# Optimization experiments

Hardware: AMD Instinct MI355X
Metric: run time of the kernel (lower is better)

## Reference

```python
import jax, jax.numpy as jnp
import numpy as np

T, B, IN, OUT = 32, 16, 64, 64
L, W, S = 4096, 64, 3          # mem_length, mem_width, shifting_size
READ_SIZE = W + 3 + S           # k, beta, g, gamma, s
WRITE_SIZE = W + 3 + S + 2 * W  # addressing params + erase + add


def setup_inputs() -> dict:
    key = jax.random.key(0)
    k1, k2 = jax.random.split(key)
    inputs = jax.random.normal(k1, (T, B, IN), dtype=jnp.float32)
    Wc = jax.random.normal(k2, (IN + OUT + W, OUT + READ_SIZE + WRITE_SIZE), dtype=jnp.float32) * 0.05
    bc = jnp.zeros((OUT + READ_SIZE + WRITE_SIZE,), dtype=jnp.float32)
    return {"inputs": inputs, "Wc": Wc, "bc": bc}


def _get_w(params, w_prev, memory):
    # params: [B, W+3+S]; w_prev: [B, L]; memory: [B, L, W]
    k = params[:, :W]
    beta = jax.nn.softplus(params[:, W])[:, None]
    g = jax.nn.sigmoid(params[:, W + 1])[:, None]
    gamma = jax.nn.softplus(params[:, W + 2])[:, None] + 1.0
    s = jax.nn.softmax(params[:, -S:], axis=-1)
    eps = 1e-14
    norm_k = jnp.sqrt(jnp.sum(k * k, axis=-1, keepdims=True) + eps)    # [B,1]
    norm_mem = jnp.sqrt(jnp.sum(memory * memory, axis=-1) + eps)       # [B,L]
    K = jnp.einsum('blw,bw->bl', memory, k) / (norm_mem * norm_k)      # cosine sim
    w_c = jax.nn.softmax(K * beta, axis=-1)
    w_g = w_c * g + (1.0 - g) * w_prev
    # circular shift: w_tilde[i] = sum_j s[j] * w_g[(i + j - left) mod L]
    left = S // 2
    shifted = jnp.stack([jnp.roll(w_g, left - j, axis=1) for j in range(S)], axis=-1)  # [B,L,S]
    w_tilde = jnp.einsum('bls,bs->bl', shifted, s)
    w = jnp.power(w_tilde, gamma)   # sharpen, gamma >= 1
    return w / jnp.sum(w, axis=1, keepdims=True)


def reference(inputs, Wc, bc):
    Bsz = inputs.shape[1]
    r0 = jnp.zeros((Bsz, W), jnp.float32)
    o0 = jnp.zeros((Bsz, OUT), jnp.float32)
    w0 = jnp.zeros((Bsz, L), jnp.float32).at[:, 0].set(1.0)  # one-hot init weights
    m0 = jnp.zeros((Bsz, L, W), jnp.float32)

    def step(carry, x_t):
        r, out, rw, ww, mem = carry
        co = jnp.concatenate([x_t, out, r], axis=1) @ Wc + bc  # linear controller
        out = co[:, :OUT]
        rp = co[:, OUT:OUT + READ_SIZE]
        wp = co[:, -WRITE_SIZE:]
        # read head (uses pre-write memory)
        rw = _get_w(rp, rw, mem)
        r = jnp.einsum('blw,bl->bw', mem, rw)
        # write head: address with same memory, then erase/add
        ww = _get_w(wp[:, :-2 * W], ww, mem)
        e = jax.nn.sigmoid(wp[:, -2 * W:-W])
        a = wp[:, -W:]
        mem = mem * (1.0 - ww[:, :, None] * e[:, None, :]) + ww[:, :, None] * a[:, None, :]
        return (r, out, rw, ww, mem), out

    _, outs = jax.lax.scan(step, (r0, o0, w0, w0, m0), inputs)
    return outs  # [T, B, OUT]
```

## Files before the change

### kernel.cpp

```cpp
#include <hip/hip_runtime.h>

#define T_STEPS 32
#define BATCH   16
#define NBPB    8
#define NBLK    (BATCH * NBPB)
#define NTHR    1024
#define LSL     512
#define MSTR    65
#define NIN     192
#define CO      332

#define OFF_CTR   0
#define OFF_SSUM  512
#define OFF_RSUM  (OFF_SSUM + BATCH * T_STEPS * 4)
#define OFF_HE    (OFF_RSUM + BATCH * T_STEPS * 64)
#define OFF_HP    (OFF_HE + BATCH * T_STEPS * NBPB * 4)
#define COMM_FLOATS (OFF_HP + BATCH * (T_STEPS + 1) * NBPB * 4)

__device__ __forceinline__ float waveSum(float v) {
#pragma unroll
  for (int off = 32; off > 0; off >>= 1) v += __shfl_xor(v, off, 64);
  return v;
}
__device__ __forceinline__ float sigmoidf(float x) { return 1.f / (1.f + __expf(-x)); }
__device__ __forceinline__ float softplusf(float x) { return x > 15.f ? x : log1pf(__expf(x)); }
__device__ __forceinline__ float aload(const float* p) {
  return __hip_atomic_load(p, __ATOMIC_RELAXED, __HIP_MEMORY_SCOPE_AGENT);
}
__device__ __forceinline__ void astore(float* p, float v) {
  __hip_atomic_store(p, v, __ATOMIC_RELAXED, __HIP_MEMORY_SCOPE_AGENT);
}

__device__ __forceinline__ void gbar(unsigned* c, unsigned expected) {
  __syncthreads();
  if (threadIdx.x == 0) {
    atomicAdd(c, 1u);
    while (__hip_atomic_load(c, __ATOMIC_RELAXED, __HIP_MEMORY_SCOPE_AGENT) < expected)
      __builtin_amdgcn_s_sleep(2);
  }
  __syncthreads();
}

__global__ void __launch_bounds__(NTHR, 1) ntm_kernel(
    const float* __restrict__ inp, const float* __restrict__ Wc,
    const float* __restrict__ bcv, float* __restrict__ dout,
    float* __restrict__ comm)
{
  const int b   = blockIdx.x >> 3;
  const int g   = blockIdx.x & 7;
  const int tid = threadIdx.x;
  const int wv  = tid >> 6;
  const int lane = tid & 63;

  __shared__ float mem[LSL * MSTR];
  __shared__ float wpR[LSL], wpW[LSL];
  __shared__ float wbR[LSL], wbW[LSL];
  __shared__ float erR[LSL], erW[LSL];
  __shared__ float xin[NIN], kr[64], kw[64], psc[12], elds[64], alds[64];
  __shared__ float outb[2][64], scrA[8], scrB[8], red[8], rpart[64], edge[8];

  unsigned* ctr = (unsigned*)comm + b * 32;

  for (int i = tid; i < LSL * MSTR; i += NTHR) mem[i] = 0.f;
  if (tid < LSL) { wpR[tid] = 0.f; wpW[tid] = 0.f; }
  if (g == 0 && tid == 0) { wpR[0] = 1.f; wpW[0] = 1.f; }
  if (tid < 64) { outb[0][tid] = 0.f; outb[1][tid] = 0.f; }
  {
    float* hp0 = comm + OFF_HP + ((size_t)(b * (T_STEPS + 1) + 0) * NBPB + g) * 4;
    if (tid == 0)       { float v = (g == 0) ? 1.f : 0.f; astore(hp0 + 0, v); astore(hp0 + 2, v); }
    if (tid == LSL - 1) { astore(hp0 + 1, 0.f); astore(hp0 + 3, 0.f); }
  }
  unsigned expct = NBPB;
  gbar(ctr, expct);

  for (int t = 0; t < T_STEPS; ++t) {
    float* sS  = comm + OFF_SSUM + (size_t)(b * T_STEPS + t) * 4;
    float* rS  = comm + OFF_RSUM + (size_t)(b * T_STEPS + t) * 64;
    float* hE  = comm + OFF_HE + ((size_t)(b * T_STEPS + t) * NBPB + g) * 4;
    float* hPn = comm + OFF_HP + ((size_t)(b * (T_STEPS + 1) + t + 1) * NBPB + g) * 4;

    if (tid < 64)       xin[tid] = inp[((size_t)t * BATCH + b) * 64 + tid];
    else if (tid < 128) xin[tid] = outb[(t + 1) & 1][tid - 64];
    else if (tid < 192) xin[tid] = (t == 0) ? 0.f
                        : aload(comm + OFF_RSUM + (size_t)(b * T_STEPS + t - 1) * 64 + (tid - 128));
    __syncthreads();

    if (tid < 2 * CO) {
      const int col = tid >> 1, h = tid & 1;
      float acc = h ? 0.f : bcv[col];
      const float* wcp = Wc + col + (size_t)(96 * h) * CO;
#pragma unroll 8
      for (int i = 0; i < 96; ++i) acc = fmaf(xin[96 * h + i], wcp[(size_t)i * CO], acc);
      acc += __shfl_xor(acc, 1, 64);
      if (h == 0) {
        if (col < 64) {
          outb[t & 1][col] = acc;
          if (g == 0) dout[((size_t)t * BATCH + b) * 64 + col] = acc;
        }
        else if (col < 128) kr[col - 64] = acc;
        else if (col < 134) psc[col - 128] = acc;
        else if (col < 198) kw[col - 134] = acc;
        else if (col < 204) psc[6 + (col - 198)] = acc;
        else if (col < 268) elds[col - 204] = sigmoidf(acc);
        else                alds[col - 268] = acc;
      }
    }
    __syncthreads();
    if (wv == 0)      { float v = kr[lane]; float s = waveSum(v * v); if (!lane) red[4] = 1.f / sqrtf(s + 1e-14f); }
    else if (wv == 1) { float v = kw[lane]; float s = waveSum(v * v); if (!lane) red[5] = 1.f / sqrtf(s + 1e-14f); }
    __syncthreads();

    {
      float sRl = 0.f, sWl = 0.f;
      if (tid < LSL) {
        const float invnkR = red[4], betaR = softplusf(psc[0]);
        const float invnkW = red[5], betaW = softplusf(psc[6]);
        float ss = 0.f, dr = 0.f, dw = 0.f;
        const int base = tid * MSTR;
#pragma unroll 8
        for (int w = 0; w < 64; ++w) {
          float v = mem[base + w];
          ss = fmaf(v, v, ss); dr = fmaf(v, kr[w], dr); dw = fmaf(v, kw[w], dw);
        }
        float rinv = rsqrtf(ss + 1e-14f);
        float eRv = __expf(betaR * (dr * rinv * invnkR - 1.f));
        float eWv = __expf(betaW * (dw * rinv * invnkW - 1.f));
        erR[tid] = eRv; erW[tid] = eWv;
        if (tid == 0)       { astore(hE + 0, eRv); astore(hE + 2, eWv); }
        if (tid == LSL - 1) { astore(hE + 1, eRv); astore(hE + 3, eWv); }
        sRl = eRv; sWl = eWv;
      }
      sRl = waveSum(sRl); sWl = waveSum(sWl);
      if (!lane && wv < 8) { scrA[wv] = sRl; scrB[wv] = sWl; }
      __syncthreads();
      if (tid == 0) {
        float a = 0.f, bb = 0.f;
        for (int j = 0; j < 8; ++j) { a += scrA[j]; bb += scrB[j]; }
        atomicAdd(sS + 0, a); atomicAdd(sS + 1, bb);
      }
    }
    expct += NBPB; gbar(ctr, expct);

    {
      const int gm = (g + NBPB - 1) & 7, gp = (g + 1) & 7;
      const float* hEm = comm + OFF_HE + ((size_t)(b * T_STEPS + t) * NBPB + gm) * 4;
      const float* hEp = comm + OFF_HE + ((size_t)(b * T_STEPS + t) * NBPB + gp) * 4;
      const float* hPm = comm + OFF_HP + ((size_t)(b * (T_STEPS + 1) + t) * NBPB + gm) * 4;
      const float* hPp = comm + OFF_HP + ((size_t)(b * (T_STEPS + 1) + t) * NBPB + gp) * 4;
      if (tid == 0) { red[0] = 1.f / aload(sS + 0); red[1] = 1.f / aload(sS + 1); }
      if (tid == 1) { edge[0] = aload(hEm + 1); edge[1] = aload(hEm + 3);
                      edge[2] = aload(hPm + 1); edge[3] = aload(hPm + 3); }
      if (tid == 2) { edge[4] = aload(hEp + 0); edge[5] = aload(hEp + 2);
                      edge[6] = aload(hPp + 0); edge[7] = aload(hPp + 2); }
      __syncthreads();

      float pRl = 0.f, pWl = 0.f;
      if (tid < LSL) {
        const float invSR = red[0], invSW = red[1];
        float gR = sigmoidf(psc[1]), gaR = softplusf(psc[2]) + 1.f;
        float x0 = psc[3], x1 = psc[4], x2 = psc[5];
        float mx = fmaxf(x0, fmaxf(x1, x2));
        float e0 = __expf(x0 - mx), e1 = __expf(x1 - mx), e2 = __expf(x2 - mx);
        float es = 1.f / (e0 + e1 + e2);
        float sr0 = e0 * es, sr1 = e1 * es, sr2 = e2 * es;
        float gW = sigmoidf(psc[7]), gaW = softplusf(psc[8]) + 1.f;
        float y0 = psc[9], y1 = psc[10], y2 = psc[11];
        float my = fmaxf(y0, fmaxf(y1, y2));
        float f0 = __expf(y0 - my), f1 = __expf(y1 - my), f2 = __expf(y2 - my);
        float fs = 1.f / (f0 + f1 + f2);
        float sw0 = f0 * fs, sw1 = f1 * fs, sw2 = f2 * fs;
        const float aR = gR * invSR, bR = 1.f - gR;
        const float aW = gW * invSW, bW = 1.f - gW;

        float erm = tid ? erR[tid - 1] : edge[0];
        float ewm = tid ? erW[tid - 1] : edge[1];
        float prm = tid ? wpR[tid - 1] : edge[2];
        float pwm = tid ? wpW[tid - 1] : edge[3];
        float erp = (tid < LSL - 1) ? erR[tid + 1] : edge[4];
        float ewp = (tid < LSL - 1) ? erW[tid + 1] : edge[5];
        float prp = (tid < LSL - 1) ? wpR[tid + 1] : edge[6];
        float pwp = (tid < LSL - 1) ? wpW[tid + 1] : edge[7];

        float wgm = aR * erm + bR * prm;
        float wg0 = aR * erR[tid] + bR * wpR[tid];
        float wgp = aR * erp + bR * prp;
        float wR = __powf(sr0 * wgm + sr1 * wg0 + sr2 * wgp, gaR);
        float vgm = aW * ewm + bW * pwm;
        float vg0 = aW * erW[tid] + bW * wpW[tid];
        float vgp = aW * ewp + bW * pwp;
        float wW = __powf(sw0 * vgm + sw1 * vg0 + sw2 * vgp, gaW);
        wbR[tid] = wR; wbW[tid] = wW;
        pRl = wR; pWl = wW;
      }
      pRl = waveSum(pRl); pWl = waveSum(pWl);
      if (!lane && wv < 8) { scrA[wv] = pRl; scrB[wv] = pWl; }
      __syncthreads();
      if (tid == 0) {
        float a = 0.f, bb = 0.f;
        for (int j = 0; j < 8; ++j) { a += scrA[j]; bb += scrB[j]; }
        atomicAdd(sS + 2, a); atomicAdd(sS + 3, bb);
      }
    }
    expct += NBPB; gbar(ctr, expct);

    {
      if (tid == 0) { red[2] = 1.f / aload(sS + 2); red[3] = 1.f / aload(sS + 3); }
      __syncthreads();
      if (tid < LSL) {
        float nR = wbR[tid] * red[2];
        float nW = wbW[tid] * red[3];
        wpR[tid] = nR; wpW[tid] = nW;
        if (tid == 0)       { astore(hPn + 0, nR); astore(hPn + 2, nW); }
        if (tid == LSL - 1) { astore(hPn + 1, nR); astore(hPn + 3, nW); }
      }
      __syncthreads();

      float rwv[8], wwv[8];
#pragma unroll
      for (int k = 0; k < 8; ++k) { rwv[k] = wpR[lane + 64 * k]; wwv[k] = wpW[lane + 64 * k]; }
#pragma unroll
      for (int r2 = 0; r2 < 4; ++r2) {
        const int w = wv * 4 + r2;
        const float e_w = elds[w], a_w = alds[w];
        float racc = 0.f;
#pragma unroll
        for (int k = 0; k < 8; ++k) {
          const int idx = (lane + 64 * k) * MSTR + w;
          float v = mem[idx];
          racc = fmaf(v, rwv[k], racc);
          float nv = fmaf(v, -(wwv[k] * e_w), v);
          mem[idx] = fmaf(wwv[k], a_w, nv);
        }
        racc = waveSum(racc);
        if (!lane) rpart[w] = racc;
      }
      __syncthreads();
      if (tid < 64) atomicAdd(rS + tid, rpart[tid]);
    }
    expct += NBPB; gbar(ctr, expct);
  }
}

extern "C" void kernel_launch(void* const* d_in, const int* in_sizes, int n_in,
                              void* d_out, int out_size, void* d_ws, size_t ws_size,
                              hipStream_t stream) {
  const float* inp = (const float*)d_in[0];
  const float* Wc  = (const float*)d_in[1];
  const float* bcv = (const float*)d_in[2];
  float* dout = (float*)d_out;
  float* comm = (float*)d_ws;

  hipMemsetAsync(comm, 0, (size_t)COMM_FLOATS * sizeof(float), stream);

  void* args[] = { (void*)&inp, (void*)&Wc, (void*)&bcv, (void*)&dout, (void*)&comm };
  hipLaunchCooperativeKernel((void*)ntm_kernel, dim3(NBLK), dim3(NTHR),
                             args, 0, stream);
}
```

Measured before the change: 753.8 us.

## Move read-vector reduction before normalization to drop one grid barrier per step

The read vector is now computed from the unnormalized sharpened weights during the second phase and divided by the global sum in the next step's controller input, which removes the third grid barrier per timestep. The similarity pass splits each row across two threads so all 1024 threads participate, and the scalar gate/shift coefficients are computed once by a single thread and broadcast through shared memory. The block-to-(batch, slice) mapping is transposed and the barrier spin sleep is shortened. The memory update now runs without a barrier after it, relying on the next step's barriers for ordering, which is a subtle correctness risk.

```diff
diff --git a/kernel.cpp b/kernel.cpp
--- a/kernel.cpp
+++ b/kernel.cpp
@@ -36,7 +36,7 @@
   if (threadIdx.x == 0) {
     atomicAdd(c, 1u);
     while (__hip_atomic_load(c, __ATOMIC_RELAXED, __HIP_MEMORY_SCOPE_AGENT) < expected)
-      __builtin_amdgcn_s_sleep(2);
+      __builtin_amdgcn_s_sleep(1);
   }
   __syncthreads();
 }
@@ -46,8 +46,8 @@
     const float* __restrict__ bcv, float* __restrict__ dout,
     float* __restrict__ comm)
 {
-  const int b   = blockIdx.x >> 3;
-  const int g   = blockIdx.x & 7;
+  const int b   = blockIdx.x & 15;
+  const int g   = blockIdx.x >> 4;
   const int tid = threadIdx.x;
   const int wv  = tid >> 6;
   const int lane = tid & 63;
@@ -57,7 +57,8 @@
   __shared__ float wbR[LSL], wbW[LSL];
   __shared__ float erR[LSL], erW[LSL];
   __shared__ float xin[NIN], kr[64], kw[64], psc[12], elds[64], alds[64];
-  __shared__ float outb[2][64], scrA[8], scrB[8], red[8], rpart[64], edge[8];
+  __shared__ float outb[2][64], scrA[16], scrB[16], red[8], rpart[64];
+  __shared__ float edge[8], coef[12];
 
   unsigned* ctr = (unsigned*)comm + b * 32;
 
@@ -81,8 +82,14 @@
 
     if (tid < 64)       xin[tid] = inp[((size_t)t * BATCH + b) * 64 + tid];
     else if (tid < 128) xin[tid] = outb[(t + 1) & 1][tid - 64];
-    else if (tid < 192) xin[tid] = (t == 0) ? 0.f
-                        : aload(comm + OFF_RSUM + (size_t)(b * T_STEPS + t - 1) * 64 + (tid - 128));
+    else if (tid < 192) {
+      if (t == 0) xin[tid] = 0.f;
+      else {
+        const float* sP = comm + OFF_SSUM + (size_t)(b * T_STEPS + t - 1) * 4;
+        const float* rP = comm + OFF_RSUM + (size_t)(b * T_STEPS + t - 1) * 64;
+        xin[tid] = aload(rP + (tid - 128)) / aload(sP + 2);
+      }
+    }
     __syncthreads();
 
     if (tid < 2 * CO) {
@@ -108,34 +115,40 @@
     __syncthreads();
     if (wv == 0)      { float v = kr[lane]; float s = waveSum(v * v); if (!lane) red[4] = 1.f / sqrtf(s + 1e-14f); }
     else if (wv == 1) { float v = kw[lane]; float s = waveSum(v * v); if (!lane) red[5] = 1.f / sqrtf(s + 1e-14f); }
+    else if (wv == 2 && !lane) { red[6] = softplusf(psc[0]); red[7] = softplusf(psc[6]); }
     __syncthreads();
 
     {
-      float sRl = 0.f, sWl = 0.f;
-      if (tid < LSL) {
-        const float invnkR = red[4], betaR = softplusf(psc[0]);
-        const float invnkW = red[5], betaW = softplusf(psc[6]);
-        float ss = 0.f, dr = 0.f, dw = 0.f;
-        const int base = tid * MSTR;
+      const float invnkR = red[4], invnkW = red[5];
+      const float betaR = red[6], betaW = red[7];
+      const int l = tid >> 1, h = tid & 1;
+      const int base = l * MSTR + 32 * h;
+      const float* krh = kr + 32 * h;
+      const float* kwh = kw + 32 * h;
+      float ss = 0.f, dr = 0.f, dw = 0.f;
 #pragma unroll 8
-        for (int w = 0; w < 64; ++w) {
-          float v = mem[base + w];
-          ss = fmaf(v, v, ss); dr = fmaf(v, kr[w], dr); dw = fmaf(v, kw[w], dw);
-        }
-        float rinv = rsqrtf(ss + 1e-14f);
-        float eRv = __expf(betaR * (dr * rinv * invnkR - 1.f));
-        float eWv = __expf(betaW * (dw * rinv * invnkW - 1.f));
-        erR[tid] = eRv; erW[tid] = eWv;
-        if (tid == 0)       { astore(hE + 0, eRv); astore(hE + 2, eWv); }
-        if (tid == LSL - 1) { astore(hE + 1, eRv); astore(hE + 3, eWv); }
-        sRl = eRv; sWl = eWv;
-      }
+      for (int i = 0; i < 32; ++i) {
+        float v = mem[base + i];
+        ss = fmaf(v, v, ss); dr = fmaf(v, krh[i], dr); dw = fmaf(v, kwh[i], dw);
+      }
+      ss += __shfl_xor(ss, 1, 64);
+      dr += __shfl_xor(dr, 1, 64);
+      dw += __shfl_xor(dw, 1, 64);
+      float rinv = rsqrtf(ss + 1e-14f);
+      float eRv = __expf(betaR * (dr * rinv * invnkR - 1.f));
+      float eWv = __expf(betaW * (dw * rinv * invnkW - 1.f));
+      if (h == 0) {
+        erR[l] = eRv; erW[l] = eWv;
+        if (l == 0)       { astore(hE + 0, eRv); astore(hE + 2, eWv); }
+        if (l == LSL - 1) { astore(hE + 1, eRv); astore(hE + 3, eWv); }
+      }
+      float sRl = h ? 0.f : eRv, sWl = h ? 0.f : eWv;
       sRl = waveSum(sRl); sWl = waveSum(sWl);
-      if (!lane && wv < 8) { scrA[wv] = sRl; scrB[wv] = sWl; }
+      if (!lane) { scrA[wv] = sRl; scrB[wv] = sWl; }
       __syncthreads();
       if (tid == 0) {
         float a = 0.f, bb = 0.f;
-        for (int j = 0; j < 8; ++j) { a += scrA[j]; bb += scrB[j]; }
+        for (int j = 0; j < 16; ++j) { a += scrA[j]; bb += scrB[j]; }
         atomicAdd(sS + 0, a); atomicAdd(sS + 1, bb);
       }
     }
@@ -143,34 +156,43 @@
 
     {
       const int gm = (g + NBPB - 1) & 7, gp = (g + 1) & 7;
-      const float* hEm = comm + OFF_HE + ((size_t)(b * T_STEPS + t) * NBPB + gm) * 4;
-      const float* hEp = comm + OFF_HE + ((size_t)(b * T_STEPS + t) * NBPB + gp) * 4;
-      const float* hPm = comm + OFF_HP + ((size_t)(b * (T_STEPS + 1) + t) * NBPB + gm) * 4;
-      const float* hPp = comm + OFF_HP + ((size_t)(b * (T_STEPS + 1) + t) * NBPB + gp) * 4;
-      if (tid == 0) { red[0] = 1.f / aload(sS + 0); red[1] = 1.f / aload(sS + 1); }
-      if (tid == 1) { edge[0] = aload(hEm + 1); edge[1] = aload(hEm + 3);
-                      edge[2] = aload(hPm + 1); edge[3] = aload(hPm + 3); }
-      if (tid == 2) { edge[4] = aload(hEp + 0); edge[5] = aload(hEp + 2);
-                      edge[6] = aload(hPp + 0); edge[7] = aload(hPp + 2); }
-      __syncthreads();
-
-      float pRl = 0.f, pWl = 0.f;
-      if (tid < LSL) {
-        const float invSR = red[0], invSW = red[1];
-        float gR = sigmoidf(psc[1]), gaR = softplusf(psc[2]) + 1.f;
+      if (tid == 0) {
+        float invSR = 1.f / aload(sS + 0), invSW = 1.f / aload(sS + 1);
+        float gR = sigmoidf(psc[1]); coef[0] = gR * invSR; coef[1] = 1.f - gR;
+        coef[2] = softplusf(psc[2]) + 1.f;
         float x0 = psc[3], x1 = psc[4], x2 = psc[5];
         float mx = fmaxf(x0, fmaxf(x1, x2));
         float e0 = __expf(x0 - mx), e1 = __expf(x1 - mx), e2 = __expf(x2 - mx);
         float es = 1.f / (e0 + e1 + e2);
-        float sr0 = e0 * es, sr1 = e1 * es, sr2 = e2 * es;
-        float gW = sigmoidf(psc[7]), gaW = softplusf(psc[8]) + 1.f;
+        coef[3] = e0 * es; coef[4] = e1 * es; coef[5] = e2 * es;
+        float gW = sigmoidf(psc[7]); coef[6] = gW * invSW; coef[7] = 1.f - gW;
+        coef[8] = softplusf(psc[8]) + 1.f;
         float y0 = psc[9], y1 = psc[10], y2 = psc[11];
         float my = fmaxf(y0, fmaxf(y1, y2));
         float f0 = __expf(y0 - my), f1 = __expf(y1 - my), f2 = __expf(y2 - my);
         float fs = 1.f / (f0 + f1 + f2);
-        float sw0 = f0 * fs, sw1 = f1 * fs, sw2 = f2 * fs;
-        const float aR = gR * invSR, bR = 1.f - gR;
-        const float aW = gW * invSW, bW = 1.f - gW;
+        coef[9] = f0 * fs; coef[10] = f1 * fs; coef[11] = f2 * fs;
+      }
+      if (tid == 1) {
+        const float* hEm = comm + OFF_HE + ((size_t)(b * T_STEPS + t) * NBPB + gm) * 4;
+        const float* hPm = comm + OFF_HP + ((size_t)(b * (T_STEPS + 1) + t) * NBPB + gm) * 4;
+        edge[0] = aload(hEm + 1); edge[1] = aload(hEm + 3);
+        edge[2] = aload(hPm + 1); edge[3] = aload(hPm + 3);
+      }
+      if (tid == 2) {
+        const float* hEp = comm + OFF_HE + ((size_t)(b * T_STEPS + t) * NBPB + gp) * 4;
+        const float* hPp = comm + OFF_HP + ((size_t)(b * (T_STEPS + 1) + t) * NBPB + gp) * 4;
+        edge[4] = aload(hEp + 0); edge[5] = aload(hEp + 2);
+        edge[6] = aload(hPp + 0); edge[7] = aload(hPp + 2);
+      }
+      __syncthreads();
+
+      float pRl = 0.f, pWl = 0.f;
+      if (tid < LSL) {
+        const float aR = coef[0], bR = coef[1], gaR = coef[2];
+        const float sr0 = coef[3], sr1 = coef[4], sr2 = coef[5];
+        const float aW = coef[6], bW = coef[7], gaW = coef[8];
+        const float sw0 = coef[9], sw1 = coef[10], sw2 = coef[11];
 
         float erm = tid ? erR[tid - 1] : edge[0];
         float ewm = tid ? erW[tid - 1] : edge[1];
@@ -200,6 +222,21 @@
         for (int j = 0; j < 8; ++j) { a += scrA[j]; bb += scrB[j]; }
         atomicAdd(sS + 2, a); atomicAdd(sS + 3, bb);
       }
+      float wbv[8];
+#pragma unroll
+      for (int k = 0; k < 8; ++k) wbv[k] = wbR[lane + 64 * k];
+#pragma unroll
+      for (int r2 = 0; r2 < 4; ++r2) {
+        const int w = wv * 4 + r2;
+        float racc = 0.f;
+#pragma unroll
+        for (int k = 0; k < 8; ++k)
+          racc = fmaf(mem[(lane + 64 * k) * MSTR + w], wbv[k], racc);
+        racc = waveSum(racc);
+        if (!lane) rpart[w] = racc;
+      }
+      __syncthreads();
+      if (tid < 64) atomicAdd(rS + tid, rpart[tid]);
     }
     expct += NBPB; gbar(ctr, expct);
 
@@ -214,30 +251,22 @@
         if (tid == LSL - 1) { astore(hPn + 1, nR); astore(hPn + 3, nW); }
       }
       __syncthreads();
-
-      float rwv[8], wwv[8];
-#pragma unroll
-      for (int k = 0; k < 8; ++k) { rwv[k] = wpR[lane + 64 * k]; wwv[k] = wpW[lane + 64 * k]; }
+      float wwv[8];
+#pragma unroll
+      for (int k = 0; k < 8; ++k) wwv[k] = wpW[lane + 64 * k];
 #pragma unroll
       for (int r2 = 0; r2 < 4; ++r2) {
         const int w = wv * 4 + r2;
         const float e_w = elds[w], a_w = alds[w];
-        float racc = 0.f;
 #pragma unroll
         for (int k = 0; k < 8; ++k) {
           const int idx = (lane + 64 * k) * MSTR + w;
           float v = mem[idx];
-          racc = fmaf(v, rwv[k], racc);
           float nv = fmaf(v, -(wwv[k] * e_w), v);
           mem[idx] = fmaf(wwv[k], a_w, nv);
         }
-        racc = waveSum(racc);
-        if (!lane) rpart[w] = racc;
-      }
-      __syncthreads();
-      if (tid < 64) atomicAdd(rS + tid, rpart[tid]);
-    }
-    expct += NBPB; gbar(ctr, expct);
+      }
+    }
   }
 }
 
```

New measurement: 710.8 us. -5.7%, faster.
